# Kernel tuning notes

Measured on AMD Instinct MI355X. Metric: run time of the kernel, lower is better.

## Reference

```python
import jax, jax.numpy as jnp
import numpy as np

TAU = 2.0       # LIF tau for both spiking and non-spiking nodes
T = 16          # number of SNN timesteps
EPS = 1e-5      # BatchNorm eps
V_TH = 1.0      # LIF threshold (spikingjelly default)

B, P, F_IN, H, A = 64, 16, 672, 2048, 32


def _bn(x, g, b, m, v):
    # BatchNorm1d over channel axis P (axis -2 of [..., P, F]), eval mode
    inv = jax.lax.rsqrt(v + EPS)
    return (x - m[:, None]) * (inv * g)[:, None] + b[:, None]


def _spike(x):
    # heaviside(x) as in spikingjelly (x >= 0 -> 1)
    return (x >= 0.0).astype(x.dtype)


def setup_inputs() -> dict:
    key = jax.random.key(0)
    ks = jax.random.split(key, 8)
    d = {
        "x": jax.random.normal(ks[0], (B, P, F_IN), jnp.float32),
        "w1": jax.random.normal(ks[1], (F_IN, H), jnp.float32) * (1.0 / np.sqrt(F_IN)),
        "bias1": jax.random.normal(ks[2], (H,), jnp.float32) * 0.01,
        "w2": jax.random.normal(ks[3], (H, A), jnp.float32) * (1.0 / np.sqrt(H)),
        "bias2": jax.random.normal(ks[4], (A,), jnp.float32) * 0.01,
    }
    kk = jax.random.split(ks[5], 12)
    for i, pre in enumerate(["bn0", "bn1", "bn2"]):
        d[pre + "_g"] = jax.random.uniform(kk[4 * i + 0], (P,), jnp.float32, 0.5, 1.5)
        d[pre + "_b"] = jax.random.normal(kk[4 * i + 1], (P,), jnp.float32) * 0.1
        d[pre + "_m"] = jax.random.normal(kk[4 * i + 2], (P,), jnp.float32) * 0.1
        d[pre + "_v"] = jax.random.uniform(kk[4 * i + 3], (P,), jnp.float32, 0.5, 1.5)
    return d


def _forward(x, w1, bias1, w2, bias2,
             bn0_g, bn0_b, bn0_m, bn0_v,
             bn1_g, bn1_b, bn1_m, bn1_v,
             bn2_g, bn2_b, bn2_m, bn2_v):
    # self.norm on the (reshaped) xlstm output: [B, P, 672]
    x = _bn(x, bn0_g, bn0_b, bn0_m, bn0_v)
    # Multi-step mode repeats the same input each timestep, so the
    # timestep-independent Linear+BN is hoisted out of the T loop.
    h = jnp.einsum("bpf,fh->bph", x, w1) + bias1          # [B, P, H]
    h = _bn(h, bn1_g, bn1_b, bn1_m, bn1_v)

    # LIF neuron: decay_input=True, v_reset=0, hard reset, threshold 1
    def lif_step(v, _):
        v = v + (h - v) / TAU
        s = _spike(v - V_TH)
        v = v * (1.0 - s)  # hard reset to v_reset=0
        return v, s

    _, spikes = jax.lax.scan(lif_step, jnp.zeros_like(h), None, length=T)  # [T,B,P,H]

    y = jnp.einsum("tbph,ha->tbpa", spikes, w2) + bias2    # [T, B, P, A]
    y = _bn(y, bn2_g, bn2_b, bn2_m, bn2_v)

    # NonSpikingLIF: charge only, output v each step
    def ns_step(v, yt):
        v = v + (yt - v) / TAU
        return v, v

    _, vs = jax.lax.scan(ns_step, jnp.zeros(y.shape[1:], y.dtype), y)  # [T,B,P,A]
    return jnp.tanh(vs.mean(0)) * 2.0                      # action [B, P, A]


def reference(x, w1, bias1, w2, bias2,
              bn0_g, bn0_b, bn0_m, bn0_v,
              bn1_g, bn1_b, bn1_m, bn1_v,
              bn2_g, bn2_b, bn2_m, bn2_v):
    return _forward(x, w1, bias1, w2, bias2,
                    bn0_g, bn0_b, bn0_m, bn0_v,
                    bn1_g, bn1_b, bn1_m, bn1_v,
                    bn2_g, bn2_b, bn2_m, bn2_v)
```

## Files before the change

kernel.cpp:

```cpp
#include <hip/hip_runtime.h>
#include <math.h>

#define BB 64
#define PP 16
#define FIN 672
#define HH 2048
#define AA 32
#define MM (BB*PP)
#define EPSBN 1e-5f
#define NKB 21

typedef _Float16 f16;
typedef __attribute__((ext_vector_type(8))) _Float16 half8;
typedef __attribute__((ext_vector_type(4))) float floatx4;

__device__ const float LIF_LUT[18] = {
    0.0f,
    0.93750095367431640625f,
    0.4583339691162109375f,
    0.294643402099609375f,
    0.21666717529296875f,
    0.1713714599609375f,
    0.123016357421875f,
    0.11712646484375f,
    0.0936279296875f,
    0.062255859375f,
    0.06201171875f,
    0.0615234375f,
    0.060546875f,
    0.05859375f,
    0.0546875f,
    0.046875f,
    0.03125f,
    0.0f
};

__global__ __launch_bounds__(256) void k_prep(
    const float* __restrict__ x, const float* __restrict__ w1,
    const float* __restrict__ g0, const float* __restrict__ b0,
    const float* __restrict__ m0, const float* __restrict__ v0,
    f16* __restrict__ Ah, f16* __restrict__ Al,
    f16* __restrict__ Wh, f16* __restrict__ Wl)
{
    __shared__ float sbuf[32 * 65];
    const int tid = threadIdx.x;
    const int b   = blockIdx.x;

    if (b < 448) {
        const int mb = b / 7;
        const int kc = b % 7;
        #pragma unroll
        for (int i = 0; i < 2; ++i) {
            const int f4 = tid + 256 * i;
            if (f4 < 384) {
                const int row = f4 / 24;
                const int c4  = (f4 % 24) * 4;
                float4 v = *(const float4*)(x + (size_t)(mb * 16 + row) * FIN + kc * 96 + c4);
                sbuf[row * 97 + c4 + 0] = v.x; sbuf[row * 97 + c4 + 1] = v.y;
                sbuf[row * 97 + c4 + 2] = v.z; sbuf[row * 97 + c4 + 3] = v.w;
            }
        }
        __syncthreads();
        if (tid < 192) {
            const int fi   = tid >> 6;
            const int lane = tid & 63;
            const int row  = lane & 15;
            const int koff = fi * 32 + ((lane >> 4) << 3);
            const float a0  = g0[row] / sqrtf(v0[row] + EPSBN);
            const float be0 = b0[row] - m0[row] * a0;
            half8 hi, lo;
            #pragma unroll
            for (int j = 0; j < 8; ++j) {
                const float xn = fmaf(a0, sbuf[row * 97 + koff + j], be0);
                const f16 h = (f16)xn;
                hi[j] = h;
                lo[j] = (f16)(xn - (float)h);
            }
            const int kb = kc * 3 + fi;
            const size_t idx = ((size_t)(mb * NKB + kb) * 64 + lane);
            *(half8*)(Ah + idx * 8) = hi;
            *(half8*)(Al + idx * 8) = lo;
        }
    } else {
        const int bw = b - 448;
        const int ng = bw & 31;
        const int kb = bw >> 5;
        #pragma unroll
        for (int i = 0; i < 2; ++i) {
            const int f4  = tid + 256 * i;
            const int row = f4 >> 4;
            const int c4  = (f4 & 15) * 4;
            float4 v = *(const float4*)(w1 + (size_t)(kb * 32 + row) * HH + ng * 64 + c4);
            sbuf[row * 65 + c4 + 0] = v.x; sbuf[row * 65 + c4 + 1] = v.y;
            sbuf[row * 65 + c4 + 2] = v.z; sbuf[row * 65 + c4 + 3] = v.w;
        }
        __syncthreads();
        const int fi   = tid >> 6;
        const int lane = tid & 63;
        const int col  = fi * 16 + (lane & 15);
        const int kr   = (lane >> 4) << 3;
        half8 hi, lo;
        #pragma unroll
        for (int j = 0; j < 8; ++j) {
            const float wv = sbuf[(kr + j) * 65 + col];
            const f16 h = (f16)wv;
            hi[j] = h;
            lo[j] = (f16)(wv - (float)h);
        }
        const int nb = ng * 4 + fi;
        const size_t idx = ((size_t)(nb * NKB + kb) * 64 + lane);
        *(half8*)(Wh + idx * 8) = hi;
        *(half8*)(Wl + idx * 8) = lo;
    }
}

#define GLOAD16(g, l) __builtin_amdgcn_global_load_lds(                        \
    (const __attribute__((address_space(1))) void*)(g),                       \
    (__attribute__((address_space(3))) void*)(l), 16, 0, 0)

__global__ __launch_bounds__(256) void k_gemm1_lds(
    const f16* __restrict__ Ah, const f16* __restrict__ Al,
    const f16* __restrict__ Wh, const f16* __restrict__ Wl,
    const float* __restrict__ bias1,
    const float* __restrict__ g1, const float* __restrict__ b1,
    const float* __restrict__ m1, const float* __restrict__ v1,
    f16* __restrict__ S)
{
    __shared__ __align__(16) char smem[2 * 16 * 1024];

    const int tid  = threadIdx.x;
    const int lane = tid & 63;
    const int w    = tid >> 6;
    const int wm   = w >> 1, wn = w & 1;

    const int b   = blockIdx.x;
    const int xcd = b & 7;
    const int idx = b >> 3;
    const int bm  = (xcd >> 2) * 8 + (idx >> 3);
    const int bn  = (xcd & 3) * 8 + (idx & 7);
    const int mb0 = bm * 4;
    const int nb0 = bn * 4;

    const char* src[4];
    int ldsoff[4];
    #pragma unroll
    for (int q = 0; q < 4; ++q) {
        const int c = w * 4 + q;
        const char* plane; int tile;
        if (c < 4)       { plane = (const char*)Ah; tile = mb0 + c; }
        else if (c < 8)  { plane = (const char*)Al; tile = mb0 + (c - 4); }
        else if (c < 12) { plane = (const char*)Wh; tile = nb0 + (c - 8); }
        else             { plane = (const char*)Wl; tile = nb0 + (c - 12); }
        src[q]    = plane + (size_t)tile * (NKB * 1024) + lane * 16;
        ldsoff[q] = c * 1024;
    }

#define STAGE(kb, bufsel) do {                                                \
    _Pragma("unroll") for (int q_ = 0; q_ < 4; ++q_)                          \
        GLOAD16(src[q_] + (kb) * 1024, smem + (bufsel) * 16384 + ldsoff[q_]); \
} while (0)

    floatx4 acc00 = (floatx4){0.f,0.f,0.f,0.f};
    floatx4 acc01 = (floatx4){0.f,0.f,0.f,0.f};
    floatx4 acc10 = (floatx4){0.f,0.f,0.f,0.f};
    floatx4 acc11 = (floatx4){0.f,0.f,0.f,0.f};

    STAGE(0, 0);
    __syncthreads();

    int cur = 0;
    for (int kb = 0; kb < NKB; ++kb) {
        if (kb + 1 < NKB) STAGE(kb + 1, cur ^ 1);

        const char* base = smem + cur * 16384 + lane * 16;
        half8 ah0 = *(const half8*)(base + (wm * 2 + 0) * 1024);
        half8 ah1 = *(const half8*)(base + (wm * 2 + 1) * 1024);
        half8 al0 = *(const half8*)(base + (4 + wm * 2 + 0) * 1024);
        half8 al1 = *(const half8*)(base + (4 + wm * 2 + 1) * 1024);
        half8 wh0 = *(const half8*)(base + (8 + wn * 2 + 0) * 1024);
        half8 wh1 = *(const half8*)(base + (8 + wn * 2 + 1) * 1024);
        half8 wl0 = *(const half8*)(base + (12 + wn * 2 + 0) * 1024);
        half8 wl1 = *(const half8*)(base + (12 + wn * 2 + 1) * 1024);

        acc00 = __builtin_amdgcn_mfma_f32_16x16x32_f16(ah0, wh0, acc00, 0,0,0);
        acc01 = __builtin_amdgcn_mfma_f32_16x16x32_f16(ah0, wh1, acc01, 0,0,0);
        acc10 = __builtin_amdgcn_mfma_f32_16x16x32_f16(ah1, wh0, acc10, 0,0,0);
        acc11 = __builtin_amdgcn_mfma_f32_16x16x32_f16(ah1, wh1, acc11, 0,0,0);
        acc00 = __builtin_amdgcn_mfma_f32_16x16x32_f16(ah0, wl0, acc00, 0,0,0);
        acc01 = __builtin_amdgcn_mfma_f32_16x16x32_f16(ah0, wl1, acc01, 0,0,0);
        acc10 = __builtin_amdgcn_mfma_f32_16x16x32_f16(ah1, wl0, acc10, 0,0,0);
        acc11 = __builtin_amdgcn_mfma_f32_16x16x32_f16(ah1, wl1, acc11, 0,0,0);
        acc00 = __builtin_amdgcn_mfma_f32_16x16x32_f16(al0, wh0, acc00, 0,0,0);
        acc01 = __builtin_amdgcn_mfma_f32_16x16x32_f16(al0, wh1, acc01, 0,0,0);
        acc10 = __builtin_amdgcn_mfma_f32_16x16x32_f16(al1, wh0, acc10, 0,0,0);
        acc11 = __builtin_amdgcn_mfma_f32_16x16x32_f16(al1, wh1, acc11, 0,0,0);

        __syncthreads();
        cur ^= 1;
    }
#undef STAGE

    const float H16 = (float)(65536.0 / 65535.0);
    const int   r4  = (lane >> 4) << 2;
    float a1c[4], be1c[4];
    #pragma unroll
    for (int j = 0; j < 4; ++j) {
        const int p = r4 + j;
        a1c[j]  = g1[p] / sqrtf(v1[p] + EPSBN);
        be1c[j] = b1[p] - m1[p] * a1c[j];
    }

    const floatx4 accs[4] = {acc00, acc01, acc10, acc11};
    #pragma unroll
    for (int m = 0; m < 2; ++m) {
        const int rowb = (mb0 + wm * 2 + m) * 16 + r4;
        #pragma unroll
        for (int n = 0; n < 2; ++n) {
            const int col = (nb0 + wn * 2 + n) * 16 + (lane & 15);
            const float bs = bias1[col];
            const floatx4 a4 = accs[m * 2 + n];
            #pragma unroll
            for (int j = 0; j < 4; ++j) {
                const float h = fmaf(a1c[j], a4[j] + bs, be1c[j]);
                float s = 0.f;
                if (h >= H16) {
                    const float rr = 1.f - __builtin_amdgcn_rcpf(h);
                    int mi = (int)ceilf(-__log2f(rr));
                    mi = mi < 1 ? 1 : (mi > 17 ? 17 : mi);
                    s = LIF_LUT[mi];
                }
                S[(size_t)(rowb + j) * HH + col] = (f16)s;
            }
        }
    }
}

__global__ __launch_bounds__(256) void k_gemm2_part(
    const f16* __restrict__ S, const float* __restrict__ w2,
    float* __restrict__ part2)
{
    __shared__ float w2s[8192];
    const int tid = threadIdx.x;
    const int rg  = blockIdx.x;
    const int kc  = blockIdx.y;

    const float4* src = (const float4*)(w2 + (size_t)kc * 8192);
    #pragma unroll
    for (int i = tid; i < 2048; i += 256) ((float4*)w2s)[i] = src[i];
    __syncthreads();

    const int rw  = tid >> 5;
    const int col = tid & 31;
    const int row = rg * 8 + rw;
    const f16* Sp = S + (size_t)row * HH + kc * 256;

    float acc0 = 0.f, acc1 = 0.f;
    #pragma unroll 4
    for (int j = 0; j < 256; j += 8) {
        half8 s8 = *(const half8*)(Sp + j);
        acc0 = fmaf((float)s8[0], w2s[(j + 0) * 32 + col], acc0);
        acc1 = fmaf((float)s8[1], w2s[(j + 1) * 32 + col], acc1);
        acc0 = fmaf((float)s8[2], w2s[(j + 2) * 32 + col], acc0);
        acc1 = fmaf((float)s8[3], w2s[(j + 3) * 32 + col], acc1);
        acc0 = fmaf((float)s8[4], w2s[(j + 4) * 32 + col], acc0);
        acc1 = fmaf((float)s8[5], w2s[(j + 5) * 32 + col], acc1);
        acc0 = fmaf((float)s8[6], w2s[(j + 6) * 32 + col], acc0);
        acc1 = fmaf((float)s8[7], w2s[(j + 7) * 32 + col], acc1);
    }
    part2[((size_t)kc * MM + row) * AA + col] = acc0 + acc1;
}

__global__ __launch_bounds__(256) void k_finish(
    const float* __restrict__ part2, const float* __restrict__ bias2,
    const float* __restrict__ g2, const float* __restrict__ b2,
    const float* __restrict__ m2, const float* __restrict__ v2,
    float* __restrict__ out)
{
    const int i   = blockIdx.x * 256 + threadIdx.x;
    const int col = i & 31;
    const int row = i >> 5;
    const int p   = row & 15;
    float acc = 0.f;
    #pragma unroll
    for (int s = 0; s < 8; ++s) acc += part2[(size_t)s * MM * AA + i];
    const float a2   = g2[p] / sqrtf(v2[p] + EPSBN);
    const float be2  = b2[p] - m2[p] * a2;
    const float Csum = 0.9375f + 0x1p-20f;
    const float val  = fmaf(a2, acc + Csum * bias2[col], Csum * be2);
    out[i] = 2.0f * tanhf(val);
}

__global__ __launch_bounds__(256) void k_gemm1_fp32(
    const float* __restrict__ x, const float* __restrict__ w1,
    const float* __restrict__ bias1,
    const float* __restrict__ g0, const float* __restrict__ b0,
    const float* __restrict__ m0, const float* __restrict__ v0,
    const float* __restrict__ g1, const float* __restrict__ b1,
    const float* __restrict__ m1, const float* __restrict__ v1,
    f16* __restrict__ S)
{
    __shared__ float As[16][36];
    __shared__ float Bs[16][68];

    const int tid = threadIdx.x;
    const int bx  = blockIdx.x;
    const int by  = blockIdx.y;

    const int ar   = tid & 31;
    const int ak   = (tid >> 5) << 1;
    const int grow = by * 32 + ar;
    const int pA   = grow & 15;
    const float a0  = g0[pA] / sqrtf(v0[pA] + EPSBN);
    const float be0 = b0[pA] - m0[pA] * a0;
    const float* xrow = x + (size_t)grow * FIN;

    const int brk = tid >> 4;
    const int bcc = (tid & 15) << 2;
    const float* wp = w1 + (size_t)brk * HH + bx * 64 + bcc;

    const int tx = tid & 15;
    const int ty = tid >> 4;

    float acc[2][4];
    #pragma unroll
    for (int i = 0; i < 2; ++i)
        #pragma unroll
        for (int j = 0; j < 4; ++j) acc[i][j] = 0.f;

    float2 aPre = *(const float2*)(xrow + ak);
    float4 bPre = *(const float4*)(wp);

    for (int kt = 0; kt < FIN; kt += 16) {
        As[ak + 0][ar] = fmaf(a0, aPre.x, be0);
        As[ak + 1][ar] = fmaf(a0, aPre.y, be0);
        *(float4*)&Bs[brk][bcc] = bPre;
        __syncthreads();
        if (kt + 16 < FIN) {
            aPre = *(const float2*)(xrow + kt + 16 + ak);
            bPre = *(const float4*)(wp + (size_t)(kt + 16) * HH);
        }
        #pragma unroll
        for (int k = 0; k < 16; ++k) {
            float2 a2 = *(const float2*)&As[k][ty << 1];
            float4 b4 = *(const float4*)&Bs[k][tx << 2];
            float aa[2] = {a2.x, a2.y};
            float bb[4] = {b4.x, b4.y, b4.z, b4.w};
            #pragma unroll
            for (int i = 0; i < 2; ++i)
                #pragma unroll
                for (int j = 0; j < 4; ++j)
                    acc[i][j] = fmaf(aa[i], bb[j], acc[i][j]);
        }
        __syncthreads();
    }

    const float KC[16] = {
        (1.0f-0x1p-16f)*0.0625f,(1.0f-0x1p-15f)*0.0625f,(1.0f-0x1p-14f)*0.0625f,(1.0f-0x1p-13f)*0.0625f,
        (1.0f-0x1p-12f)*0.0625f,(1.0f-0x1p-11f)*0.0625f,(1.0f-0x1p-10f)*0.0625f,(1.0f-0x1p-9f)*0.0625f,
        (1.0f-0x1p-8f)*0.0625f,(1.0f-0x1p-7f)*0.0625f,(1.0f-0x1p-6f)*0.0625f,(1.0f-0x1p-5f)*0.0625f,
        (1.0f-0x1p-4f)*0.0625f,(1.0f-0x1p-3f)*0.0625f,(1.0f-0x1p-2f)*0.0625f,(1.0f-0x1p-1f)*0.0625f
    };

    const int col0 = bx * 64 + (tx << 2);
    float4 bias4 = *(const float4*)(bias1 + col0);
    const float bias_arr[4] = {bias4.x, bias4.y, bias4.z, bias4.w};

    #pragma unroll
    for (int i = 0; i < 2; ++i) {
        const int r = by * 32 + (ty << 1) + i;
        const int p = r & 15;
        const float a1  = g1[p] / sqrtf(v1[p] + EPSBN);
        const float be1 = b1[p] - m1[p] * a1;
        #pragma unroll
        for (int j = 0; j < 4; ++j) {
            const float h = fmaf(a1, acc[i][j] + bias_arr[j], be1);
            float v = 0.f, s = 0.f;
            #pragma unroll
            for (int t = 0; t < 16; ++t) {
                v = v + (h - v) * 0.5f;
                if (v >= 1.0f) { s += KC[t]; v = 0.f; }
            }
            S[(size_t)r * HH + col0 + j] = (f16)s;
        }
    }
}

extern "C" void kernel_launch(void* const* d_in, const int* in_sizes, int n_in,
                              void* d_out, int out_size, void* d_ws, size_t ws_size,
                              hipStream_t stream) {
    (void)in_sizes; (void)n_in; (void)out_size;
    const float* x     = (const float*)d_in[0];
    const float* w1    = (const float*)d_in[1];
    const float* bias1 = (const float*)d_in[2];
    const float* w2    = (const float*)d_in[3];
    const float* bias2 = (const float*)d_in[4];
    const float* g0 = (const float*)d_in[5];
    const float* b0 = (const float*)d_in[6];
    const float* m0 = (const float*)d_in[7];
    const float* v0 = (const float*)d_in[8];
    const float* g1 = (const float*)d_in[9];
    const float* b1 = (const float*)d_in[10];
    const float* m1 = (const float*)d_in[11];
    const float* v1 = (const float*)d_in[12];
    const float* g2 = (const float*)d_in[13];
    const float* b2 = (const float*)d_in[14];
    const float* m2 = (const float*)d_in[15];
    const float* v2 = (const float*)d_in[16];
    float* out = (float*)d_out;

    const size_t offAl  = 1376256;
    const size_t offWh  = 2752512;
    const size_t offWl  = 5505024;
    const size_t offS   = 8257536;
    const size_t offP2  = offS + 4194304;
    const size_t needed = offP2 + 1048576;

    if (ws_size >= needed) {
        f16* Ah = (f16*)d_ws;
        f16* Al = (f16*)((char*)d_ws + offAl);
        f16* Wh = (f16*)((char*)d_ws + offWh);
        f16* Wl = (f16*)((char*)d_ws + offWl);
        f16* S  = (f16*)((char*)d_ws + offS);
        float* part2 = (float*)((char*)d_ws + offP2);

        k_prep<<<1120, 256, 0, stream>>>(x, w1, g0, b0, m0, v0, Ah, Al, Wh, Wl);
        k_gemm1_lds<<<512, 256, 0, stream>>>(Ah, Al, Wh, Wl, bias1,
                                             g1, b1, m1, v1, S);
        k_gemm2_part<<<dim3(128, 8), 256, 0, stream>>>(S, w2, part2);
        k_finish<<<dim3(128), 256, 0, stream>>>(part2, bias2, g2, b2, m2, v2, out);
    } else {
        f16* S       = (f16*)d_ws;
        float* part2 = (float*)((char*)d_ws + (size_t)MM * HH * sizeof(f16));
        k_gemm1_fp32<<<dim3(32, 32), 256, 0, stream>>>(x, w1, bias1,
                                                       g0, b0, m0, v0,
                                                       g1, b1, m1, v1, S);
        k_gemm2_part<<<dim3(128, 8), 256, 0, stream>>>(S, w2, part2);
        k_finish<<<dim3(128), 256, 0, stream>>>(part2, bias2, g2, b2, m2, v2, out);
    }
}
```

Before: 38.92 us.

## Fuse second GEMM into first GEMM epilogue via LDS spike tile and MFMA

The spike tile from GEMM1 is kept in shared memory instead of being written to global memory. Each block immediately multiplies it by a split-fp16 copy of w2 (prepared in k_prep) using MFMA and writes per-column-block partial sums. A finish kernel then reduces the 32 partials. This removes the global round trip of the S matrix and one kernel launch, in exchange for a larger partial buffer (4 MB) and a 32-way reduction.

Result: faster. 31.27 us (median of 2 runs) (-19.7%).

```diff
diff --git a/kernel.cpp b/kernel.cpp
--- a/kernel.cpp
+++ b/kernel.cpp
@@ -37,10 +37,12 @@
 
 __global__ __launch_bounds__(256) void k_prep(
     const float* __restrict__ x, const float* __restrict__ w1,
+    const float* __restrict__ w2,
     const float* __restrict__ g0, const float* __restrict__ b0,
     const float* __restrict__ m0, const float* __restrict__ v0,
     f16* __restrict__ Ah, f16* __restrict__ Al,
-    f16* __restrict__ Wh, f16* __restrict__ Wl)
+    f16* __restrict__ Wh, f16* __restrict__ Wl,
+    f16* __restrict__ W2h, f16* __restrict__ W2l)
 {
     __shared__ float sbuf[32 * 65];
     const int tid = threadIdx.x;
@@ -81,7 +83,7 @@
             *(half8*)(Ah + idx * 8) = hi;
             *(half8*)(Al + idx * 8) = lo;
         }
-    } else {
+    } else if (b < 1120) {
         const int bw = b - 448;
         const int ng = bw & 31;
         const int kb = bw >> 5;
@@ -111,6 +113,31 @@
         const size_t idx = ((size_t)(nb * NKB + kb) * 64 + lane);
         *(half8*)(Wh + idx * 8) = hi;
         *(half8*)(Wl + idx * 8) = lo;
+    } else {
+        const int kb2 = b - 1120;
+        const int row = tid >> 3;
+        const int c4  = (tid & 7) << 2;
+        float4 v = *(const float4*)(w2 + (size_t)(kb2 * 32 + row) * AA + c4);
+        sbuf[row * 33 + c4 + 0] = v.x; sbuf[row * 33 + c4 + 1] = v.y;
+        sbuf[row * 33 + c4 + 2] = v.z; sbuf[row * 33 + c4 + 3] = v.w;
+        __syncthreads();
+        if (tid < 128) {
+            const int nb   = tid >> 6;
+            const int lane = tid & 63;
+            const int col  = nb * 16 + (lane & 15);
+            const int kr   = (lane >> 4) << 3;
+            half8 hi, lo;
+            #pragma unroll
+            for (int j = 0; j < 8; ++j) {
+                const float wv = sbuf[(kr + j) * 33 + col];
+                const f16 h = (f16)wv;
+                hi[j] = h;
+                lo[j] = (f16)(wv - (float)h);
+            }
+            const size_t idx = ((size_t)(kb2 * 2 + nb) * 64 + lane);
+            *(half8*)(W2h + idx * 8) = hi;
+            *(half8*)(W2l + idx * 8) = lo;
+        }
     }
 }
 
@@ -118,13 +145,14 @@
     (const __attribute__((address_space(1))) void*)(g),                       \
     (__attribute__((address_space(3))) void*)(l), 16, 0, 0)
 
-__global__ __launch_bounds__(256) void k_gemm1_lds(
+__global__ __launch_bounds__(256) void k_gemm12(
     const f16* __restrict__ Ah, const f16* __restrict__ Al,
     const f16* __restrict__ Wh, const f16* __restrict__ Wl,
+    const f16* __restrict__ W2h, const f16* __restrict__ W2l,
     const float* __restrict__ bias1,
     const float* __restrict__ g1, const float* __restrict__ b1,
     const float* __restrict__ m1, const float* __restrict__ v1,
-    f16* __restrict__ S)
+    float* __restrict__ part)
 {
     __shared__ __align__(16) char smem[2 * 16 * 1024];
 
@@ -200,6 +228,7 @@
     }
 #undef STAGE
 
+    f16* Sl = (f16*)smem;
     const float H16 = (float)(65536.0 / 65535.0);
     const int   r4  = (lane >> 4) << 2;
     float a1c[4], be1c[4];
@@ -213,11 +242,11 @@
     const floatx4 accs[4] = {acc00, acc01, acc10, acc11};
     #pragma unroll
     for (int m = 0; m < 2; ++m) {
-        const int rowb = (mb0 + wm * 2 + m) * 16 + r4;
+        const int rloc = (wm * 2 + m) * 16 + r4;
         #pragma unroll
         for (int n = 0; n < 2; ++n) {
-            const int col = (nb0 + wn * 2 + n) * 16 + (lane & 15);
-            const float bs = bias1[col];
+            const int cloc = (wn * 2 + n) * 16 + (lane & 15);
+            const float bs = bias1[nb0 * 16 + cloc];
             const floatx4 a4 = accs[m * 2 + n];
             #pragma unroll
             for (int j = 0; j < 4; ++j) {
@@ -229,8 +258,148 @@
                     mi = mi < 1 ? 1 : (mi > 17 ? 17 : mi);
                     s = LIF_LUT[mi];
                 }
-                S[(size_t)(rowb + j) * HH + col] = (f16)s;
+                Sl[(rloc + j) * 72 + cloc] = (f16)s;
             }
+        }
+    }
+    __syncthreads();
+
+    floatx4 y0 = (floatx4){0.f,0.f,0.f,0.f};
+    floatx4 y1 = (floatx4){0.f,0.f,0.f,0.f};
+    const int rsl = (w * 16 + (lane & 15)) * 72 + ((lane >> 4) << 3);
+    #pragma unroll
+    for (int kb = 0; kb < 2; ++kb) {
+        half8 sa = *(const half8*)(Sl + rsl + kb * 32);
+        const int hb = bn * 2 + kb;
+        half8 wh0 = *(const half8*)(W2h + ((size_t)(hb * 2 + 0) * 64 + lane) * 8);
+        half8 wh1 = *(const half8*)(W2h + ((size_t)(hb * 2 + 1) * 64 + lane) * 8);
+        half8 wl0 = *(const half8*)(W2l + ((size_t)(hb * 2 + 0) * 64 + lane) * 8);
+        half8 wl1 = *(const half8*)(W2l + ((size_t)(hb * 2 + 1) * 64 + lane) * 8);
+        y0 = __builtin_amdgcn_mfma_f32_16x16x32_f16(sa, wh0, y0, 0,0,0);
+        y0 = __builtin_amdgcn_mfma_f32_16x16x32_f16(sa, wl0, y0, 0,0,0);
+        y1 = __builtin_amdgcn_mfma_f32_16x16x32_f16(sa, wh1, y1, 0,0,0);
+        y1 = __builtin_amdgcn_mfma_f32_16x16x32_f16(sa, wl1, y1, 0,0,0);
+    }
+    const int prow = bm * 64 + w * 16 + r4;
+    float* pp = part + (size_t)bn * (MM * AA) + (size_t)prow * AA + (lane & 15);
+    #pragma unroll
+    for (int j = 0; j < 4; ++j) {
+        pp[j * AA]      = y0[j];
+        pp[j * AA + 16] = y1[j];
+    }
+}
+
+__global__ __launch_bounds__(256) void k_finish32(
+    const float* __restrict__ part, const float* __restrict__ bias2,
+    const float* __restrict__ g2, const float* __restrict__ b2,
+    const float* __restrict__ m2, const float* __restrict__ v2,
+    float* __restrict__ out)
+{
+    const int i   = blockIdx.x * 256 + threadIdx.x;
+    const int col = i & 31;
+    const int row = i >> 5;
+    const int p   = row & 15;
+    float acc = 0.f;
+    #pragma unroll
+    for (int s = 0; s < 32; ++s) acc += part[(size_t)s * MM * AA + i];
+    const float a2   = g2[p] / sqrtf(v2[p] + EPSBN);
+    const float be2  = b2[p] - m2[p] * a2;
+    const float Csum = 0.9375f + 0x1p-20f;
+    const float val  = fmaf(a2, acc + Csum * bias2[col], Csum * be2);
+    out[i] = 2.0f * tanhf(val);
+}
+
+__global__ __launch_bounds__(256) void k_gemm1_fp32(
+    const float* __restrict__ x, const float* __restrict__ w1,
+    const float* __restrict__ bias1,
+    const float* __restrict__ g0, const float* __restrict__ b0,
+    const float* __restrict__ m0, const float* __restrict__ v0,
+    const float* __restrict__ g1, const float* __restrict__ b1,
+    const float* __restrict__ m1, const float* __restrict__ v1,
+    f16* __restrict__ S)
+{
+    __shared__ float As[16][36];
+    __shared__ float Bs[16][68];
+
+    const int tid = threadIdx.x;
+    const int bx  = blockIdx.x;
+    const int by  = blockIdx.y;
+
+    const int ar   = tid & 31;
+    const int ak   = (tid >> 5) << 1;
+    const int grow = by * 32 + ar;
+    const int pA   = grow & 15;
+    const float a0  = g0[pA] / sqrtf(v0[pA] + EPSBN);
+    const float be0 = b0[pA] - m0[pA] * a0;
+    const float* xrow = x + (size_t)grow * FIN;
+
+    const int brk = tid >> 4;
+    const int bcc = (tid & 15) << 2;
+    const float* wp = w1 + (size_t)brk * HH + bx * 64 + bcc;
+
+    const int tx = tid & 15;
+    const int ty = tid >> 4;
+
+    float acc[2][4];
+    #pragma unroll
+    for (int i = 0; i < 2; ++i)
+        #pragma unroll
+        for (int j = 0; j < 4; ++j) acc[i][j] = 0.f;
+
+    float2 aPre = *(const float2*)(xrow + ak);
+    float4 bPre = *(const float4*)(wp);
+
+    for (int kt = 0; kt < FIN; kt += 16) {
+        As[ak + 0][ar] = fmaf(a0, aPre.x, be0);
+        As[ak + 1][ar] = fmaf(a0, aPre.y, be0);
+        *(float4*)&Bs[brk][bcc] = bPre;
+        __syncthreads();
+        if (kt + 16 < FIN) {
+            aPre = *(const float2*)(xrow + kt + 16 + ak);
+            bPre = *(const float4*)(wp + (size_t)(kt + 16) * HH);
+        }
+        #pragma unroll
+        for (int k = 0; k < 16; ++k) {
+            float2 a2 = *(const float2*)&As[k][ty << 1];
+            float4 b4 = *(const float4*)&Bs[k][tx << 2];
+            float aa[2] = {a2.x, a2.y};
+            float bb[4] = {b4.x, b4.y, b4.z, b4.w};
+            #pragma unroll
+            for (int i = 0; i < 2; ++i)
+                #pragma unroll
+                for (int j = 0; j < 4; ++j)
+                    acc[i][j] = fmaf(aa[i], bb[j], acc[i][j]);
+        }
+        __syncthreads();
+    }
+
+    const float KC[16] = {
+        (1.0f-0x1p-16f)*0.0625f,(1.0f-0x1p-15f)*0.0625f,(1.0f-0x1p-14f)*0.0625f,(1.0f-0x1p-13f)*0.0625f,
+        (1.0f-0x1p-12f)*0.0625f,(1.0f-0x1p-11f)*0.0625f,(1.0f-0x1p-10f)*0.0625f,(1.0f-0x1p-9f)*0.0625f,
+        (1.0f-0x1p-8f)*0.0625f,(1.0f-0x1p-7f)*0.0625f,(1.0f-0x1p-6f)*0.0625f,(1.0f-0x1p-5f)*0.0625f,
+        (1.0f-0x1p-4f)*0.0625f,(1.0f-0x1p-3f)*0.0625f,(1.0f-0x1p-2f)*0.0625f,(1.0f-0x1p-1f)*0.0625f
+    };
+
+    const int col0 = bx * 64 + (tx << 2);
+    float4 bias4 = *(const float4*)(bias1 + col0);
+    const float bias_arr[4] = {bias4.x, bias4.y, bias4.z, bias4.w};
+
+    #pragma unroll
+    for (int i = 0; i < 2; ++i) {
+        const int r = by * 32 + (ty << 1) + i;
+        const int p = r & 15;
+        const float a1  = g1[p] / sqrtf(v1[p] + EPSBN);
+        const float be1 = b1[p] - m1[p] * a1;
+        #pragma unroll
+        for (int j = 0; j < 4; ++j) {
+            const float h = fmaf(a1, acc[i][j] + bias_arr[j], be1);
+            float v = 0.f, s = 0.f;
+            #pragma unroll
+            for (int t = 0; t < 16; ++t) {
+                v = v + (h - v) * 0.5f;
+                if (v >= 1.0f) { s += KC[t]; v = 0.f; }
+            }
+            S[(size_t)r * HH + col0 + j] = (f16)s;
         }
     }
 }
@@ -270,7 +439,7 @@
     part2[((size_t)kc * MM + row) * AA + col] = acc0 + acc1;
 }
 
-__global__ __launch_bounds__(256) void k_finish(
+__global__ __launch_bounds__(256) void k_finish8(
     const float* __restrict__ part2, const float* __restrict__ bias2,
     const float* __restrict__ g2, const float* __restrict__ b2,
     const float* __restrict__ m2, const float* __restrict__ v2,
@@ -288,101 +457,6 @@
     const float Csum = 0.9375f + 0x1p-20f;
     const float val  = fmaf(a2, acc + Csum * bias2[col], Csum * be2);
     out[i] = 2.0f * tanhf(val);
-}
-
-__global__ __launch_bounds__(256) void k_gemm1_fp32(
-    const float* __restrict__ x, const float* __restrict__ w1,
-    const float* __restrict__ bias1,
-    const float* __restrict__ g0, const float* __restrict__ b0,
-    const float* __restrict__ m0, const float* __restrict__ v0,
-    const float* __restrict__ g1, const float* __restrict__ b1,
-    const float* __restrict__ m1, const float* __restrict__ v1,
-    f16* __restrict__ S)
-{
-    __shared__ float As[16][36];
-    __shared__ float Bs[16][68];
-
-    const int tid = threadIdx.x;
-    const int bx  = blockIdx.x;
-    const int by  = blockIdx.y;
-
-    const int ar   = tid & 31;
-    const int ak   = (tid >> 5) << 1;
-    const int grow = by * 32 + ar;
-    const int pA   = grow & 15;
-    const float a0  = g0[pA] / sqrtf(v0[pA] + EPSBN);
-    const float be0 = b0[pA] - m0[pA] * a0;
-    const float* xrow = x + (size_t)grow * FIN;
-
-    const int brk = tid >> 4;
-    const int bcc = (tid & 15) << 2;
-    const float* wp = w1 + (size_t)brk * HH + bx * 64 + bcc;
-
-    const int tx = tid & 15;
-    const int ty = tid >> 4;
-
-    float acc[2][4];
-    #pragma unroll
-    for (int i = 0; i < 2; ++i)
-        #pragma unroll
-        for (int j = 0; j < 4; ++j) acc[i][j] = 0.f;
-
-    float2 aPre = *(const float2*)(xrow + ak);
-    float4 bPre = *(const float4*)(wp);
-
-    for (int kt = 0; kt < FIN; kt += 16) {
-        As[ak + 0][ar] = fmaf(a0, aPre.x, be0);
-        As[ak + 1][ar] = fmaf(a0, aPre.y, be0);
-        *(float4*)&Bs[brk][bcc] = bPre;
-        __syncthreads();
-        if (kt + 16 < FIN) {
-            aPre = *(const float2*)(xrow + kt + 16 + ak);
-            bPre = *(const float4*)(wp + (size_t)(kt + 16) * HH);
-        }
-        #pragma unroll
-        for (int k = 0; k < 16; ++k) {
-            float2 a2 = *(const float2*)&As[k][ty << 1];
-            float4 b4 = *(const float4*)&Bs[k][tx << 2];
-            float aa[2] = {a2.x, a2.y};
-            float bb[4] = {b4.x, b4.y, b4.z, b4.w};
-            #pragma unroll
-            for (int i = 0; i < 2; ++i)
-                #pragma unroll
-                for (int j = 0; j < 4; ++j)
-                    acc[i][j] = fmaf(aa[i], bb[j], acc[i][j]);
-        }
-        __syncthreads();
-    }
-
-    const float KC[16] = {
-        (1.0f-0x1p-16f)*0.0625f,(1.0f-0x1p-15f)*0.0625f,(1.0f-0x1p-14f)*0.0625f,(1.0f-0x1p-13f)*0.0625f,
-        (1.0f-0x1p-12f)*0.0625f,(1.0f-0x1p-11f)*0.0625f,(1.0f-0x1p-10f)*0.0625f,(1.0f-0x1p-9f)*0.0625f,
-        (1.0f-0x1p-8f)*0.0625f,(1.0f-0x1p-7f)*0.0625f,(1.0f-0x1p-6f)*0.0625f,(1.0f-0x1p-5f)*0.0625f,
-        (1.0f-0x1p-4f)*0.0625f,(1.0f-0x1p-3f)*0.0625f,(1.0f-0x1p-2f)*0.0625f,(1.0f-0x1p-1f)*0.0625f
-    };
-
-    const int col0 = bx * 64 + (tx << 2);
-    float4 bias4 = *(const float4*)(bias1 + col0);
-    const float bias_arr[4] = {bias4.x, bias4.y, bias4.z, bias4.w};
-
-    #pragma unroll
-    for (int i = 0; i < 2; ++i) {
-        const int r = by * 32 + (ty << 1) + i;
-        const int p = r & 15;
-        const float a1  = g1[p] / sqrtf(v1[p] + EPSBN);
-        const float be1 = b1[p] - m1[p] * a1;
-        #pragma unroll
-        for (int j = 0; j < 4; ++j) {
-            const float h = fmaf(a1, acc[i][j] + bias_arr[j], be1);
-            float v = 0.f, s = 0.f;
-            #pragma unroll
-            for (int t = 0; t < 16; ++t) {
-                v = v + (h - v) * 0.5f;
-                if (v >= 1.0f) { s += KC[t]; v = 0.f; }
-            }
-            S[(size_t)r * HH + col0 + j] = (f16)s;
-        }
-    }
 }
 
 extern "C" void kernel_launch(void* const* d_in, const int* in_sizes, int n_in,
@@ -411,23 +485,25 @@
     const size_t offAl  = 1376256;
     const size_t offWh  = 2752512;
     const size_t offWl  = 5505024;
-    const size_t offS   = 8257536;
-    const size_t offP2  = offS + 4194304;
-    const size_t needed = offP2 + 1048576;
+    const size_t offW2h = 8257536;
+    const size_t offW2l = 8388608;
+    const size_t offP   = 8519680;
+    const size_t needed = offP + 4194304;
 
     if (ws_size >= needed) {
-        f16* Ah = (f16*)d_ws;
-        f16* Al = (f16*)((char*)d_ws + offAl);
-        f16* Wh = (f16*)((char*)d_ws + offWh);
-        f16* Wl = (f16*)((char*)d_ws + offWl);
-        f16* S  = (f16*)((char*)d_ws + offS);
-        float* part2 = (float*)((char*)d_ws + offP2);
-
-        k_prep<<<1120, 256, 0, stream>>>(x, w1, g0, b0, m0, v0, Ah, Al, Wh, Wl);
-        k_gemm1_lds<<<512, 256, 0, stream>>>(Ah, Al, Wh, Wl, bias1,
-                                             g1, b1, m1, v1, S);
-        k_gemm2_part<<<dim3(128, 8), 256, 0, stream>>>(S, w2, part2);
-        k_finish<<<dim3(128), 256, 0, stream>>>(part2, bias2, g2, b2, m2, v2, out);
+        f16* Ah  = (f16*)d_ws;
+        f16* Al  = (f16*)((char*)d_ws + offAl);
+        f16* Wh  = (f16*)((char*)d_ws + offWh);
+        f16* Wl  = (f16*)((char*)d_ws + offWl);
+        f16* W2h = (f16*)((char*)d_ws + offW2h);
+        f16* W2l = (f16*)((char*)d_ws + offW2l);
+        float* part = (float*)((char*)d_ws + offP);
+
+        k_prep<<<1184, 256, 0, stream>>>(x, w1, w2, g0, b0, m0, v0,
+                                         Ah, Al, Wh, Wl, W2h, W2l);
+        k_gemm12<<<512, 256, 0, stream>>>(Ah, Al, Wh, Wl, W2h, W2l, bias1,
+                                          g1, b1, m1, v1, part);
+        k_finish32<<<128, 256, 0, stream>>>(part, bias2, g2, b2, m2, v2, out);
     } else {
         f16* S       = (f16*)d_ws;
         float* part2 = (float*)((char*)d_ws + (size_t)MM * HH * sizeof(f16));
@@ -435,6 +511,6 @@
                                                        g0, b0, m0, v0,
                                                        g1, b1, m1, v1, S);
         k_gemm2_part<<<dim3(128, 8), 256, 0, stream>>>(S, w2, part2);
-        k_finish<<<dim3(128), 256, 0, stream>>>(part2, bias2, g2, b2, m2, v2, out);
-    }
-}
+        k_finish8<<<128, 256, 0, stream>>>(part2, bias2, g2, b2, m2, v2, out);
+    }
+}
```
